# Optimization experiments

Measured on AMD Instinct MI355X. Metric: run time of the kernel, lower is better.

Reference implementation:

```python
import jax, jax.numpy as jnp
import numpy as np

D_MODEL = 1024
NUM_EXPERTS = 8


def setup_inputs() -> dict:
    key = jax.random.key(0)
    k_x, k_wg, k_bg, k_we, k_be = jax.random.split(key, 5)
    B, S, D, E = 4, 2048, D_MODEL, NUM_EXPERTS
    x = jax.random.normal(k_x, (B, S, D), dtype=jnp.float32)
    # gate: nn.Linear(d_model, num_experts) -> weight [E, D], bias [E]
    Wg = jax.random.normal(k_wg, (E, D), dtype=jnp.float32) * 0.02
    bg = jax.random.normal(k_bg, (E,), dtype=jnp.float32) * 0.02
    # experts: E x nn.Linear(d_model, d_model) -> weights [E, D, D], biases [E, D]
    We = jax.random.normal(k_we, (E, D, D), dtype=jnp.float32) * 0.02
    be = jax.random.normal(k_be, (E, D), dtype=jnp.float32) * 0.02
    return {"x": x, "Wg": Wg, "bg": bg, "We": We, "be": be, "top_k": 2}


def reference(x, Wg, bg, We, be, top_k):
    # gate_scores: softmax over experts. x:[B,S,D], Wg:[E,D] -> [B,S,E]
    gate_scores = jax.nn.softmax(jnp.einsum("bsd,ed->bse", x, Wg) + bg, axis=-1)
    top_k_values, top_k_indices = jax.lax.top_k(gate_scores, top_k)  # [B,S,K]
    # dense all-expert compute (faithful to original): [B,S,D,E]
    expert_outputs = jnp.einsum("bsd,ekd->bske", x, We) + be.T  # be.T: [D,E]
    # gather top-k experts along last dim: idx broadcast over feature dim D
    top_k_outputs = jnp.take_along_axis(
        expert_outputs, top_k_indices[:, :, None, :], axis=-1
    )  # [B,S,D,K]
    weighted = (top_k_outputs * top_k_values[:, :, None, :]).sum(axis=-1)  # [B,S,D]
    return weighted
```

## Files before the change

kernel.cpp:

```cpp
#include <hip/hip_runtime.h>
#include <hip/hip_bf16.h>
#include <stdint.h>

#define D_MODEL 1024
#define NUM_EXPERTS 8
#define NBUCKET 16
#define BM 128
#define BN 128
#define BK 64
#define KSTEPS (D_MODEL / BK)
#define GATE_TOK 32

typedef __bf16 bf16x8 __attribute__((ext_vector_type(8)));
typedef float f32x4 __attribute__((ext_vector_type(4)));
typedef unsigned short u16x8 __attribute__((ext_vector_type(8)));

__device__ __forceinline__ unsigned short f32_to_bf16_rne(float f) {
    union { float f; uint32_t u; } v;
    v.f = f;
    uint32_t u = v.u;
    u += 0x7FFFu + ((u >> 16) & 1u);
    return (unsigned short)(u >> 16);
}

__device__ __forceinline__ float bf16_to_f32(unsigned short h) {
    union { uint32_t u; float f; } v;
    v.u = ((uint32_t)h) << 16;
    return v.f;
}

__device__ __forceinline__ void gload_lds16(const unsigned short* g, unsigned short* l) {
    __builtin_amdgcn_global_load_lds(
        (const __attribute__((address_space(1))) void*)g,
        (__attribute__((address_space(3))) void*)l,
        16, 0, 0);
}

__global__ __launch_bounds__(256) void gate_kernel(
    const float* __restrict__ x, const float* __restrict__ Wg,
    const float* __restrict__ bg, int T,
    int* __restrict__ counts, int* __restrict__ token_list,
    float* __restrict__ gate_list, unsigned short* __restrict__ xb)
{
    const int tid  = threadIdx.x;
    const int lane = tid & 63;
    const int wave = tid >> 6;
    const int tokBase = blockIdx.x * GATE_TOK;

    __shared__ float4 WgS[NUM_EXPERTS * 256];
    __shared__ double logitS[GATE_TOK][NUM_EXPERTS];
    __shared__ int cntS[NBUCKET];
    __shared__ int baseS[NBUCKET];

    if (tid < NBUCKET) cntS[tid] = 0;
#pragma unroll
    for (int i = 0; i < 8; i++)
        WgS[i * 256 + tid] = ((const float4*)Wg)[i * 256 + tid];
    __syncthreads();

    for (int tt = 0; tt < GATE_TOK / 4; tt++) {
        const int lt = wave * (GATE_TOK / 4) + tt;
        const int token = tokBase + lt;
        const float4* xr4 = (const float4*)(x + (size_t)token * D_MODEL);
        ushort4* xbr4 = (ushort4*)(xb + (size_t)token * D_MODEL);

        float4 xv[4];
#pragma unroll
        for (int q = 0; q < 4; q++) {
            float4 f = xr4[q * 64 + lane];
            xv[q] = f;
            ushort4 o;
            o.x = f32_to_bf16_rne(f.x);
            o.y = f32_to_bf16_rne(f.y);
            o.z = f32_to_bf16_rne(f.z);
            o.w = f32_to_bf16_rne(f.w);
            xbr4[q * 64 + lane] = o;
        }

        double acc[NUM_EXPERTS];
#pragma unroll
        for (int e = 0; e < NUM_EXPERTS; e++) {
            double a = 0.0;
#pragma unroll
            for (int q = 0; q < 4; q++) {
                float4 w = WgS[e * 256 + q * 64 + lane];
                a += (double)xv[q].x * (double)w.x;
                a += (double)xv[q].y * (double)w.y;
                a += (double)xv[q].z * (double)w.z;
                a += (double)xv[q].w * (double)w.w;
            }
            acc[e] = a;
        }
#pragma unroll
        for (int e = 0; e < NUM_EXPERTS; e++) {
            double a = acc[e];
            for (int off = 32; off > 0; off >>= 1) a += __shfl_xor(a, off, 64);
            acc[e] = a;
        }
        if (lane == 0) {
#pragma unroll
            for (int e = 0; e < NUM_EXPERTS; e++)
                logitS[lt][e] = acc[e] + (double)bg[e];
        }
    }
    __syncthreads();

    int i1 = 0, i2 = 0, o1 = 0, o2 = 0;
    double v1d = 0.0, v2d = 0.0;
    const int token2 = tokBase + tid;
    if (tid < GATE_TOK) {
        double lg[NUM_EXPERTS];
#pragma unroll
        for (int e = 0; e < NUM_EXPERTS; e++) lg[e] = logitS[tid][e];
        i1 = 0;
#pragma unroll
        for (int e = 1; e < NUM_EXPERTS; e++) if (lg[e] > lg[i1]) i1 = e;
        i2 = (i1 == 0) ? 1 : 0;
#pragma unroll
        for (int e = 0; e < NUM_EXPERTS; e++)
            if (e != i1 && lg[e] > lg[i2]) i2 = e;
        double m = lg[i1], den = 0.0;
#pragma unroll
        for (int e = 0; e < NUM_EXPERTS; e++) den += exp(lg[e] - m);
        v1d = exp(lg[i1] - m) / den;
        v2d = exp(lg[i2] - m) / den;
        o1 = atomicAdd(&cntS[i1], 1);
        o2 = atomicAdd(&cntS[8 + i2], 1);
    }
    __syncthreads();
    if (tid < NBUCKET) baseS[tid] = atomicAdd(&counts[tid], cntS[tid]);
    __syncthreads();
    if (tid < GATE_TOK) {
        int p1 = i1 * T + baseS[i1] + o1;
        token_list[p1] = token2;
        gate_list[p1]  = (float)v1d;
        int p2 = (8 + i2) * T + baseS[8 + i2] + o2;
        token_list[p2] = token2;
        gate_list[p2]  = (float)v2d;
    }
}

__global__ __launch_bounds__(256) void convert_kernel(
    const float* __restrict__ src, unsigned short* __restrict__ dst)
{
    int gid = blockIdx.x * 256 + threadIdx.x;
    int s   = gid & 7;
    int n   = (gid >> 3) & 1023;
    int kt  = (gid >> 13) & (KSTEPS - 1);
    int e   = gid >> 17;

    const float* sp = src + ((size_t)(e * 1024 + n)) * 1024 + kt * BK + s * 8;
    float4 a = ((const float4*)sp)[0];
    float4 b = ((const float4*)sp)[1];
    u16x8 o;
    o[0] = f32_to_bf16_rne(a.x);
    o[1] = f32_to_bf16_rne(a.y);
    o[2] = f32_to_bf16_rne(a.z);
    o[3] = f32_to_bf16_rne(a.w);
    o[4] = f32_to_bf16_rne(b.x);
    o[5] = f32_to_bf16_rne(b.y);
    o[6] = f32_to_bf16_rne(b.z);
    o[7] = f32_to_bf16_rne(b.w);

    int ss = s ^ (n & 7);
    unsigned short* dp = dst + (((size_t)(e * KSTEPS + kt) * 1024 + n) * BK) + ss * 8;
    *(u16x8*)dp = o;
}

__global__ __launch_bounds__(256) void moe_gemm(
    const unsigned short* __restrict__ xb,
    const unsigned short* __restrict__ wb,
    const float* __restrict__ be,
    const int* __restrict__ counts,
    const int* __restrict__ token_list,
    const float* __restrict__ gate_list,
    unsigned short* __restrict__ ybuf,
    int T)
{
    const int bid = blockIdx.x;
    const int nt = bid & 7;
    const int rest = bid >> 3;
    const int vexp = rest & (NBUCKET - 1);
    const int mt = rest >> 4;
    const int e_w = vexp & 7;

    const int n_e = counts[vexp];
    const int m0 = mt * BM;
    if (m0 >= n_e) return;
    const int n0 = nt * BN;
    const int tid = threadIdx.x;

    __shared__ __align__(16) unsigned short As[2][BM * BK];
    __shared__ __align__(16) unsigned short Bs[2][BN * BK];
    __shared__ int   tokS[BM];
    __shared__ float gateS[BM];

    if (tid < BM) {
        int r = m0 + tid;
        int tk = 0; float gv = 0.f;
        if (r < n_e) {
            tk = token_list[vexp * T + r];
            gv = gate_list[vexp * T + r];
        }
        tokS[tid]  = tk;
        gateS[tid] = gv;
    }
    __syncthreads();

    const unsigned short* asrc[4];
#pragma unroll
    for (int i = 0; i < 4; i++) {
        int flat = i * 256 + tid;
        int r = flat >> 3, seg = flat & 7;
        int ss = seg ^ (r & 7);
        asrc[i] = xb + (size_t)tokS[r] * D_MODEL + ss * 8;
    }
    const unsigned short* bsrc =
        wb + (size_t)e_w * (KSTEPS * 1024 * BK) + (size_t)n0 * BK;

    const int wave = tid >> 6, lane = tid & 63;
    const int wm = (wave >> 1) * 64, wn = (wave & 1) * 64;
    const int frow = lane & 15;
    const int qq = lane >> 4;
    const int sw8 = frow & 7;

    f32x4 acc[4][4];
#pragma unroll
    for (int mi = 0; mi < 4; mi++)
#pragma unroll
        for (int ni = 0; ni < 4; ni++)
            acc[mi][ni] = (f32x4){0.f, 0.f, 0.f, 0.f};

#pragma unroll
    for (int i = 0; i < 4; i++) {
        int flat = i * 256 + tid;
        gload_lds16(asrc[i], &As[0][flat * 8]);
        gload_lds16(bsrc + flat * 8, &Bs[0][flat * 8]);
    }

#pragma unroll 2
    for (int kt = 0; kt < KSTEPS; kt++) {
        const int cur = kt & 1;
        if (kt + 1 < KSTEPS) {
#pragma unroll
            for (int i = 0; i < 4; i++) {
                int flat = i * 256 + tid;
                gload_lds16(asrc[i] + (kt + 1) * BK, &As[cur ^ 1][flat * 8]);
                gload_lds16(bsrc + (size_t)(kt + 1) * (1024 * BK) + flat * 8,
                            &Bs[cur ^ 1][flat * 8]);
            }
            asm volatile("s_waitcnt vmcnt(8)" ::: "memory");
        } else {
            asm volatile("s_waitcnt vmcnt(0)" ::: "memory");
        }
        __builtin_amdgcn_sched_barrier(0);
        __builtin_amdgcn_s_barrier();
        __builtin_amdgcn_sched_barrier(0);

#pragma unroll
        for (int ks = 0; ks < 2; ks++) {
            const int off = ((ks * 4 + qq) ^ sw8) * 8;
            bf16x8 af[4], bfv[4];
#pragma unroll
            for (int mi = 0; mi < 4; mi++)
                af[mi] = *(const bf16x8*)&As[cur][(wm + mi * 16 + frow) * BK + off];
#pragma unroll
            for (int ni = 0; ni < 4; ni++)
                bfv[ni] = *(const bf16x8*)&Bs[cur][(wn + ni * 16 + frow) * BK + off];
#pragma unroll
            for (int mi = 0; mi < 4; mi++)
#pragma unroll
                for (int ni = 0; ni < 4; ni++)
                    acc[mi][ni] = __builtin_amdgcn_mfma_f32_16x16x32_bf16(
                        af[mi], bfv[ni], acc[mi][ni], 0, 0, 0);
        }
        __builtin_amdgcn_sched_barrier(0);
        __builtin_amdgcn_s_barrier();
        __builtin_amdgcn_sched_barrier(0);
    }

    unsigned short* ybase = ybuf + (size_t)(vexp >> 3) * T * D_MODEL;
    const int rbase = (lane >> 4) * 4;
    const int col   = lane & 15;
#pragma unroll
    for (int mi = 0; mi < 4; mi++) {
#pragma unroll
        for (int r = 0; r < 4; r++) {
            int lrow = wm + mi * 16 + rbase + r;
            if (m0 + lrow < n_e) {
                int   tk = tokS[lrow];
                float gv = gateS[lrow];
                unsigned short* yr = ybase + (size_t)tk * D_MODEL;
#pragma unroll
                for (int ni = 0; ni < 4; ni++) {
                    int c = n0 + wn + ni * 16 + col;
                    float val = gv * (acc[mi][ni][r] + be[e_w * D_MODEL + c]);
                    yr[c] = f32_to_bf16_rne(val);
                }
            }
        }
    }
}

__global__ __launch_bounds__(256) void combine_kernel(
    const unsigned short* __restrict__ y0,
    const unsigned short* __restrict__ y1,
    float* __restrict__ out, int n4)
{
    int i = blockIdx.x * 256 + threadIdx.x;
    if (i >= n4) return;
    ushort4 a = ((const ushort4*)y0)[i];
    ushort4 b = ((const ushort4*)y1)[i];
    float4 o;
    o.x = bf16_to_f32(a.x) + bf16_to_f32(b.x);
    o.y = bf16_to_f32(a.y) + bf16_to_f32(b.y);
    o.z = bf16_to_f32(a.z) + bf16_to_f32(b.z);
    o.w = bf16_to_f32(a.w) + bf16_to_f32(b.w);
    ((float4*)out)[i] = o;
}

extern "C" void kernel_launch(void* const* d_in, const int* in_sizes, int n_in,
                              void* d_out, int out_size, void* d_ws, size_t ws_size,
                              hipStream_t stream) {
    const float* x  = (const float*)d_in[0];
    const float* Wg = (const float*)d_in[1];
    const float* bg = (const float*)d_in[2];
    const float* We = (const float*)d_in[3];
    const float* be = (const float*)d_in[4];

    const int T = in_sizes[0] / D_MODEL;

    char* ws = (char*)d_ws;
    unsigned short* xb = (unsigned short*)ws;
    size_t off = (size_t)T * D_MODEL * 2;
    unsigned short* wbv = (unsigned short*)(ws + off);
    off += (size_t)NUM_EXPERTS * D_MODEL * D_MODEL * 2;
    int* counts = (int*)(ws + off);         off += 256;
    int* token_list = (int*)(ws + off);     off += (size_t)NBUCKET * T * 4;
    float* gate_list = (float*)(ws + off);  off += (size_t)NBUCKET * T * 4;
    unsigned short* ybuf = (unsigned short*)(ws + off);
    off += (size_t)2 * T * D_MODEL * 2;

    hipMemsetAsync(counts, 0, 256, stream);

    int nseg = NUM_EXPERTS * KSTEPS * 1024 * 8;
    convert_kernel<<<nseg / 256, 256, 0, stream>>>(We, wbv);

    gate_kernel<<<T / GATE_TOK, 256, 0, stream>>>(
        x, Wg, bg, T, counts, token_list, gate_list, xb);

    const int MT = (T + BM - 1) / BM;
    moe_gemm<<<MT * NBUCKET * 8, 256, 0, stream>>>(
        xb, wbv, be, counts, token_list, gate_list, ybuf, T);

    int n4c = T * D_MODEL / 4;
    combine_kernel<<<(n4c + 255) / 256, 256, 0, stream>>>(
        ybuf, ybuf + (size_t)T * D_MODEL, (float*)d_out, n4c);
}
```

Before: 211.0 us.

## Fuse top-k combine into GEMM epilogue via two sequential expert-slot passes

The single GEMM launch over 16 buckets is split into two launches, one per top-k slot. The first writes fp32 results straight to the output and the second reads them back and accumulates in place. This removes the bf16 intermediate buffers and the separate combine kernel. The gate kernel also moves from 256 to 512 threads per block, with each wave handling fewer tokens. The cost is a second kernel launch, a serialization point between the slots, and an uncoalesced read-modify-write of fp32 output in the second pass.

```diff
diff --git a/kernel.cpp b/kernel.cpp
--- a/kernel.cpp
+++ b/kernel.cpp
@@ -23,12 +23,6 @@
     return (unsigned short)(u >> 16);
 }
 
-__device__ __forceinline__ float bf16_to_f32(unsigned short h) {
-    union { uint32_t u; float f; } v;
-    v.u = ((uint32_t)h) << 16;
-    return v.f;
-}
-
 __device__ __forceinline__ void gload_lds16(const unsigned short* g, unsigned short* l) {
     __builtin_amdgcn_global_load_lds(
         (const __attribute__((address_space(1))) void*)g,
@@ -36,7 +30,7 @@
         16, 0, 0);
 }
 
-__global__ __launch_bounds__(256) void gate_kernel(
+__global__ __launch_bounds__(512) void gate_kernel(
     const float* __restrict__ x, const float* __restrict__ Wg,
     const float* __restrict__ bg, int T,
     int* __restrict__ counts, int* __restrict__ token_list,
@@ -54,12 +48,12 @@
 
     if (tid < NBUCKET) cntS[tid] = 0;
 #pragma unroll
-    for (int i = 0; i < 8; i++)
-        WgS[i * 256 + tid] = ((const float4*)Wg)[i * 256 + tid];
-    __syncthreads();
-
-    for (int tt = 0; tt < GATE_TOK / 4; tt++) {
-        const int lt = wave * (GATE_TOK / 4) + tt;
+    for (int i = 0; i < 4; i++)
+        WgS[i * 512 + tid] = ((const float4*)Wg)[i * 512 + tid];
+    __syncthreads();
+
+    for (int tt = 0; tt < GATE_TOK / 8; tt++) {
+        const int lt = wave * (GATE_TOK / 8) + tt;
         const int token = tokBase + lt;
         const float4* xr4 = (const float4*)(x + (size_t)token * D_MODEL);
         ushort4* xbr4 = (ushort4*)(xb + (size_t)token * D_MODEL);
@@ -174,15 +168,16 @@
     const int* __restrict__ counts,
     const int* __restrict__ token_list,
     const float* __restrict__ gate_list,
-    unsigned short* __restrict__ ybuf,
-    int T)
+    float* out,
+    int T, int sec)
 {
     const int bid = blockIdx.x;
     const int nt = bid & 7;
     const int rest = bid >> 3;
-    const int vexp = rest & (NBUCKET - 1);
-    const int mt = rest >> 4;
-    const int e_w = vexp & 7;
+    const int vloc = rest & 7;
+    const int mt = rest >> 3;
+    const int vexp = sec * 8 + vloc;
+    const int e_w = vloc;
 
     const int n_e = counts[vexp];
     const int m0 = mt * BM;
@@ -279,7 +274,6 @@
         __builtin_amdgcn_sched_barrier(0);
     }
 
-    unsigned short* ybase = ybuf + (size_t)(vexp >> 3) * T * D_MODEL;
     const int rbase = (lane >> 4) * 4;
     const int col   = lane & 15;
 #pragma unroll
@@ -290,33 +284,17 @@
             if (m0 + lrow < n_e) {
                 int   tk = tokS[lrow];
                 float gv = gateS[lrow];
-                unsigned short* yr = ybase + (size_t)tk * D_MODEL;
+                float* yr = out + (size_t)tk * D_MODEL;
 #pragma unroll
                 for (int ni = 0; ni < 4; ni++) {
                     int c = n0 + wn + ni * 16 + col;
                     float val = gv * (acc[mi][ni][r] + be[e_w * D_MODEL + c]);
-                    yr[c] = f32_to_bf16_rne(val);
+                    if (sec) val += yr[c];
+                    yr[c] = val;
                 }
             }
         }
     }
-}
-
-__global__ __launch_bounds__(256) void combine_kernel(
-    const unsigned short* __restrict__ y0,
-    const unsigned short* __restrict__ y1,
-    float* __restrict__ out, int n4)
-{
-    int i = blockIdx.x * 256 + threadIdx.x;
-    if (i >= n4) return;
-    ushort4 a = ((const ushort4*)y0)[i];
-    ushort4 b = ((const ushort4*)y1)[i];
-    float4 o;
-    o.x = bf16_to_f32(a.x) + bf16_to_f32(b.x);
-    o.y = bf16_to_f32(a.y) + bf16_to_f32(b.y);
-    o.z = bf16_to_f32(a.z) + bf16_to_f32(b.z);
-    o.w = bf16_to_f32(a.w) + bf16_to_f32(b.w);
-    ((float4*)out)[i] = o;
 }
 
 extern "C" void kernel_launch(void* const* d_in, const int* in_sizes, int n_in,
@@ -338,22 +316,18 @@
     int* counts = (int*)(ws + off);         off += 256;
     int* token_list = (int*)(ws + off);     off += (size_t)NBUCKET * T * 4;
     float* gate_list = (float*)(ws + off);  off += (size_t)NBUCKET * T * 4;
-    unsigned short* ybuf = (unsigned short*)(ws + off);
-    off += (size_t)2 * T * D_MODEL * 2;
 
     hipMemsetAsync(counts, 0, 256, stream);
 
     int nseg = NUM_EXPERTS * KSTEPS * 1024 * 8;
     convert_kernel<<<nseg / 256, 256, 0, stream>>>(We, wbv);
 
-    gate_kernel<<<T / GATE_TOK, 256, 0, stream>>>(
+    gate_kernel<<<T / GATE_TOK, 512, 0, stream>>>(
         x, Wg, bg, T, counts, token_list, gate_list, xb);
 
     const int MT = (T + BM - 1) / BM;
-    moe_gemm<<<MT * NBUCKET * 8, 256, 0, stream>>>(
-        xb, wbv, be, counts, token_list, gate_list, ybuf, T);
-
-    int n4c = T * D_MODEL / 4;
-    combine_kernel<<<(n4c + 255) / 256, 256, 0, stream>>>(
-        ybuf, ybuf + (size_t)T * D_MODEL, (float*)d_out, n4c);
-}
+    moe_gemm<<<MT * 8 * 8, 256, 0, stream>>>(
+        xb, wbv, be, counts, token_list, gate_list, (float*)d_out, T, 0);
+    moe_gemm<<<MT * 8 * 8, 256, 0, stream>>>(
+        xb, wbv, be, counts, token_list, gate_list, (float*)d_out, T, 1);
+}
```

New measurement: 305.8 us. 1.45x slower.

## Fuse weight conversion into gate kernel and use 512-thread GEMM blocks

Applied to the files above, without the earlier changes.

Merges the expert-weight bf16 conversion and the gating kernel into one launch, with separate block ranges for each job. The convert path now walks the fp32 source linearly so reads coalesce, while writes are scattered into the swizzled tile layout. The grouped GEMM moves to 8 waves per block with a 2x4 wave grid, which halves the per-wave accumulator tile and the loads issued per thread. This aims to cut a launch, overlap the two prep jobs, and raise occupancy, but it reduces register-level reuse per wave and relies on GATE_BLOCKS matching T/GATE_TOK.

```diff
diff --git a/kernel.cpp b/kernel.cpp
--- a/kernel.cpp
+++ b/kernel.cpp
@@ -10,6 +10,9 @@
 #define BK 64
 #define KSTEPS (D_MODEL / BK)
 #define GATE_TOK 32
+#define GATE_BLOCKS 256
+#define CONV_BLOCKS 2048
+#define NSEG (NUM_EXPERTS * KSTEPS * 1024 * 8)
 
 typedef __bf16 bf16x8 __attribute__((ext_vector_type(8)));
 typedef float f32x4 __attribute__((ext_vector_type(4)));
@@ -36,13 +39,42 @@
         16, 0, 0);
 }
 
-__global__ __launch_bounds__(256) void gate_kernel(
+__global__ __launch_bounds__(512) void prep_kernel(
     const float* __restrict__ x, const float* __restrict__ Wg,
-    const float* __restrict__ bg, int T,
+    const float* __restrict__ bg, const float* __restrict__ We, int T,
     int* __restrict__ counts, int* __restrict__ token_list,
-    float* __restrict__ gate_list, unsigned short* __restrict__ xb)
+    float* __restrict__ gate_list, unsigned short* __restrict__ xb,
+    unsigned short* __restrict__ wbv)
 {
-    const int tid  = threadIdx.x;
+    const int tid = threadIdx.x;
+
+    if (blockIdx.x >= GATE_BLOCKS) {
+        int g = (blockIdx.x - GATE_BLOCKS) * 512 + tid;
+        int s   = g & 7;
+        int kt  = (g >> 3) & (KSTEPS - 1);
+        int n   = (g >> 7) & 1023;
+        int e   = g >> 17;
+
+        const float* sp = We + (size_t)g * 8;
+        float4 a = ((const float4*)sp)[0];
+        float4 b = ((const float4*)sp)[1];
+        u16x8 o;
+        o[0] = f32_to_bf16_rne(a.x);
+        o[1] = f32_to_bf16_rne(a.y);
+        o[2] = f32_to_bf16_rne(a.z);
+        o[3] = f32_to_bf16_rne(a.w);
+        o[4] = f32_to_bf16_rne(b.x);
+        o[5] = f32_to_bf16_rne(b.y);
+        o[6] = f32_to_bf16_rne(b.z);
+        o[7] = f32_to_bf16_rne(b.w);
+
+        int ss = s ^ (n & 7);
+        unsigned short* dp =
+            wbv + (((size_t)(e * KSTEPS + kt) * 1024 + n) * BK) + ss * 8;
+        *(u16x8*)dp = o;
+        return;
+    }
+
     const int lane = tid & 63;
     const int wave = tid >> 6;
     const int tokBase = blockIdx.x * GATE_TOK;
@@ -54,12 +86,12 @@
 
     if (tid < NBUCKET) cntS[tid] = 0;
 #pragma unroll
-    for (int i = 0; i < 8; i++)
-        WgS[i * 256 + tid] = ((const float4*)Wg)[i * 256 + tid];
-    __syncthreads();
-
-    for (int tt = 0; tt < GATE_TOK / 4; tt++) {
-        const int lt = wave * (GATE_TOK / 4) + tt;
+    for (int i = 0; i < 4; i++)
+        WgS[i * 512 + tid] = ((const float4*)Wg)[i * 512 + tid];
+    __syncthreads();
+
+    for (int tt = 0; tt < GATE_TOK / 8; tt++) {
+        const int lt = wave * (GATE_TOK / 8) + tt;
         const int token = tokBase + lt;
         const float4* xr4 = (const float4*)(x + (size_t)token * D_MODEL);
         ushort4* xbr4 = (ushort4*)(xb + (size_t)token * D_MODEL);
@@ -140,34 +172,7 @@
     }
 }
 
-__global__ __launch_bounds__(256) void convert_kernel(
-    const float* __restrict__ src, unsigned short* __restrict__ dst)
-{
-    int gid = blockIdx.x * 256 + threadIdx.x;
-    int s   = gid & 7;
-    int n   = (gid >> 3) & 1023;
-    int kt  = (gid >> 13) & (KSTEPS - 1);
-    int e   = gid >> 17;
-
-    const float* sp = src + ((size_t)(e * 1024 + n)) * 1024 + kt * BK + s * 8;
-    float4 a = ((const float4*)sp)[0];
-    float4 b = ((const float4*)sp)[1];
-    u16x8 o;
-    o[0] = f32_to_bf16_rne(a.x);
-    o[1] = f32_to_bf16_rne(a.y);
-    o[2] = f32_to_bf16_rne(a.z);
-    o[3] = f32_to_bf16_rne(a.w);
-    o[4] = f32_to_bf16_rne(b.x);
-    o[5] = f32_to_bf16_rne(b.y);
-    o[6] = f32_to_bf16_rne(b.z);
-    o[7] = f32_to_bf16_rne(b.w);
-
-    int ss = s ^ (n & 7);
-    unsigned short* dp = dst + (((size_t)(e * KSTEPS + kt) * 1024 + n) * BK) + ss * 8;
-    *(u16x8*)dp = o;
-}
-
-__global__ __launch_bounds__(256) void moe_gemm(
+__global__ __launch_bounds__(512) void moe_gemm(
     const unsigned short* __restrict__ xb,
     const unsigned short* __restrict__ wb,
     const float* __restrict__ be,
@@ -207,10 +212,10 @@
     }
     __syncthreads();
 
-    const unsigned short* asrc[4];
-#pragma unroll
-    for (int i = 0; i < 4; i++) {
-        int flat = i * 256 + tid;
+    const unsigned short* asrc[2];
+#pragma unroll
+    for (int i = 0; i < 2; i++) {
+        int flat = i * 512 + tid;
         int r = flat >> 3, seg = flat & 7;
         int ss = seg ^ (r & 7);
         asrc[i] = xb + (size_t)tokS[r] * D_MODEL + ss * 8;
@@ -219,21 +224,21 @@
         wb + (size_t)e_w * (KSTEPS * 1024 * BK) + (size_t)n0 * BK;
 
     const int wave = tid >> 6, lane = tid & 63;
-    const int wm = (wave >> 1) * 64, wn = (wave & 1) * 64;
+    const int wm = (wave >> 2) * 64, wn = (wave & 3) * 32;
     const int frow = lane & 15;
     const int qq = lane >> 4;
     const int sw8 = frow & 7;
 
-    f32x4 acc[4][4];
+    f32x4 acc[4][2];
 #pragma unroll
     for (int mi = 0; mi < 4; mi++)
 #pragma unroll
-        for (int ni = 0; ni < 4; ni++)
+        for (int ni = 0; ni < 2; ni++)
             acc[mi][ni] = (f32x4){0.f, 0.f, 0.f, 0.f};
 
 #pragma unroll
-    for (int i = 0; i < 4; i++) {
-        int flat = i * 256 + tid;
+    for (int i = 0; i < 2; i++) {
+        int flat = i * 512 + tid;
         gload_lds16(asrc[i], &As[0][flat * 8]);
         gload_lds16(bsrc + flat * 8, &Bs[0][flat * 8]);
     }
@@ -243,13 +248,13 @@
         const int cur = kt & 1;
         if (kt + 1 < KSTEPS) {
 #pragma unroll
-            for (int i = 0; i < 4; i++) {
-                int flat = i * 256 + tid;
+            for (int i = 0; i < 2; i++) {
+                int flat = i * 512 + tid;
                 gload_lds16(asrc[i] + (kt + 1) * BK, &As[cur ^ 1][flat * 8]);
                 gload_lds16(bsrc + (size_t)(kt + 1) * (1024 * BK) + flat * 8,
                             &Bs[cur ^ 1][flat * 8]);
             }
-            asm volatile("s_waitcnt vmcnt(8)" ::: "memory");
+            asm volatile("s_waitcnt vmcnt(4)" ::: "memory");
         } else {
             asm volatile("s_waitcnt vmcnt(0)" ::: "memory");
         }
@@ -260,17 +265,17 @@
 #pragma unroll
         for (int ks = 0; ks < 2; ks++) {
             const int off = ((ks * 4 + qq) ^ sw8) * 8;
-            bf16x8 af[4], bfv[4];
+            bf16x8 af[4], bfv[2];
 #pragma unroll
             for (int mi = 0; mi < 4; mi++)
                 af[mi] = *(const bf16x8*)&As[cur][(wm + mi * 16 + frow) * BK + off];
 #pragma unroll
-            for (int ni = 0; ni < 4; ni++)
+            for (int ni = 0; ni < 2; ni++)
                 bfv[ni] = *(const bf16x8*)&Bs[cur][(wn + ni * 16 + frow) * BK + off];
 #pragma unroll
             for (int mi = 0; mi < 4; mi++)
 #pragma unroll
-                for (int ni = 0; ni < 4; ni++)
+                for (int ni = 0; ni < 2; ni++)
                     acc[mi][ni] = __builtin_amdgcn_mfma_f32_16x16x32_bf16(
                         af[mi], bfv[ni], acc[mi][ni], 0, 0, 0);
         }
@@ -292,7 +297,7 @@
                 float gv = gateS[lrow];
                 unsigned short* yr = ybase + (size_t)tk * D_MODEL;
 #pragma unroll
-                for (int ni = 0; ni < 4; ni++) {
+                for (int ni = 0; ni < 2; ni++) {
                     int c = n0 + wn + ni * 16 + col;
                     float val = gv * (acc[mi][ni][r] + be[e_w * D_MODEL + c]);
                     yr[c] = f32_to_bf16_rne(val);
@@ -343,14 +348,11 @@
 
     hipMemsetAsync(counts, 0, 256, stream);
 
-    int nseg = NUM_EXPERTS * KSTEPS * 1024 * 8;
-    convert_kernel<<<nseg / 256, 256, 0, stream>>>(We, wbv);
-
-    gate_kernel<<<T / GATE_TOK, 256, 0, stream>>>(
-        x, Wg, bg, T, counts, token_list, gate_list, xb);
+    prep_kernel<<<GATE_BLOCKS + CONV_BLOCKS, 512, 0, stream>>>(
+        x, Wg, bg, We, T, counts, token_list, gate_list, xb, wbv);
 
     const int MT = (T + BM - 1) / BM;
-    moe_gemm<<<MT * NBUCKET * 8, 256, 0, stream>>>(
+    moe_gemm<<<MT * NBUCKET * 8, 512, 0, stream>>>(
         xb, wbv, be, counts, token_list, gate_list, ybuf, T);
 
     int n4c = T * D_MODEL / 4;
```

Result: slower. 231.6 us (+9.7%).
